# Kernel optimization log

Measured on AMD Instinct MI355X. Metric: run time of the kernel, lower is better.

Reference implementation:

```python
import jax, jax.numpy as jnp
import numpy as np

B, S, H, I, E, K = 2, 1024, 768, 1536, 8, 2
CAPACITY_FACTOR = 1.5
ROUTING_TEMP = 1.0
LB_WEIGHT = 0.001


def setup_inputs() -> dict:
    key = jax.random.key(0)
    k_x, k_g, k_w1, k_w3, k_w2 = jax.random.split(key, 5)
    std = 0.02
    return {
        "x": jax.random.normal(k_x, (B, S, H), dtype=jnp.float32),
        "w_gate": jax.random.normal(k_g, (H, E), dtype=jnp.float32) * 0.02,
        "w1": jax.random.normal(k_w1, (E, H, I), dtype=jnp.float32) * std,
        "w3": jax.random.normal(k_w3, (E, H, I), dtype=jnp.float32) * std,
        "w2": jax.random.normal(k_w2, (E, I, H), dtype=jnp.float32) * (std / np.sqrt(2 * 12)),
    }


def _moe_forward(x, w_gate, w1, w3, w2):
    Bb, Ss, Hh = x.shape
    T = Bb * Ss
    xf = x.reshape(T, Hh)

    # --- routing ---
    gate_logits = (xf @ w_gate) / ROUTING_TEMP          # [T, E]
    gate_probs = jax.nn.softmax(gate_logits, axis=-1)   # [T, E]
    topk_probs, topk_idx = jax.lax.top_k(gate_probs, K)  # [T, K]
    topk_probs = topk_probs / (topk_probs.sum(-1, keepdims=True) + 1e-8)

    # --- capacity dropping (per-k slot, token order, like the torch loop) ---
    capacity = max(8, int((T * K // E) * CAPACITY_FACTOR))
    onehot = (topk_idx[:, :, None] == jnp.arange(E)[None, None, :])  # [T, K, E] bool
    ranks = jnp.cumsum(onehot.astype(jnp.int32), axis=0)             # position of token in expert queue
    keep = onehot & (ranks <= capacity)                               # [T, K, E]

    # combine weight per (token, expert): sum over k of kept, clamped routing prob
    w_clamped = jnp.clip(topk_probs, 1e-8, 10.0)                      # [T, K]
    combine = jnp.einsum("tk,tke->te", w_clamped, keep.astype(xf.dtype))  # [T, E]

    # --- dense per-expert SwiGLU (reference form of masked dispatch) ---
    g = jnp.einsum("th,ehi->tei", xf, w1)   # [T, E, I]
    u = jnp.einsum("th,ehi->tei", xf, w3)   # [T, E, I]
    h = jax.nn.silu(g) * u                    # [T, E, I]
    y = jnp.einsum("tei,eih->teh", h, w2)   # [T, E, H]
    out = jnp.einsum("te,teh->th", combine, y).reshape(Bb, Ss, Hh)

    # --- load balancing loss ---
    expert_counts = keep.sum(axis=(0, 1)).astype(jnp.float32)         # [E]
    dropped = (onehot.sum() - keep.sum()).astype(jnp.float32)
    expert_usage = jax.lax.stop_gradient(expert_counts) / float(max(T * K, 1))
    gate_importance = gate_probs.mean(axis=0)                          # [E]
    aux = jnp.sum(expert_usage * gate_importance) * E
    aux = aux + jnp.where(dropped > 0, dropped / float(max(T, 1)) * 0.1, 0.0)
    aux = jnp.minimum(aux, 1.0) * LB_WEIGHT
    return out, aux


def reference(x, w_gate, w1, w3, w2):
    return _moe_forward(x, w_gate, w1, w3, w2)
```

## Files before the change

### kernel.cpp

```cpp
#include <hip/hip_runtime.h>
#include <math.h>

#define T_TOK 2048
#define HD 768
#define ID 1536
#define NE 8
#define CAP 768
#define TK 4096

typedef __bf16 bf16_t;
typedef __bf16 bf16x8 __attribute__((ext_vector_type(8)));
typedef __bf16 bf16x4 __attribute__((ext_vector_type(4)));
typedef float floatx4 __attribute__((ext_vector_type(4)));

__device__ __forceinline__ void gld16(const bf16_t* g, bf16_t* l) {
  __builtin_amdgcn_global_load_lds(
      (__attribute__((address_space(1))) void*)(g),
      (__attribute__((address_space(3))) void*)(l),
      16, 0, 0);
}

__global__ void k_route(const float* __restrict__ x, const float* __restrict__ wg,
                        bf16_t* __restrict__ xbf, int2* __restrict__ idx2,
                        float2* __restrict__ wc2, int2* __restrict__ tok_rows,
                        float* __restrict__ imp) {
  int t = blockIdx.x * 4 + (threadIdx.x >> 6);
  int lane = threadIdx.x & 63;
  const float* xr = x + (size_t)t * HD;
  int off = lane * 12;
  float4 a = *(const float4*)(xr + off);
  float4 b = *(const float4*)(xr + off + 4);
  float4 c = *(const float4*)(xr + off + 8);
  float xv[12] = {a.x, a.y, a.z, a.w, b.x, b.y, b.z, b.w, c.x, c.y, c.z, c.w};
  bf16x4 s0, s1, s2;
#pragma unroll
  for (int j = 0; j < 4; ++j) { s0[j] = (bf16_t)xv[j]; s1[j] = (bf16_t)xv[4 + j]; s2[j] = (bf16_t)xv[8 + j]; }
  bf16_t* xo = xbf + (size_t)t * HD + off;
  *(bf16x4*)xo = s0; *(bf16x4*)(xo + 4) = s1; *(bf16x4*)(xo + 8) = s2;

  float acc[8] = {0, 0, 0, 0, 0, 0, 0, 0};
#pragma unroll
  for (int jj = 0; jj < 12; ++jj) {
    const float4* wr = (const float4*)(wg + (size_t)(off + jj) * 8);
    float4 w0 = wr[0], w1 = wr[1];
    float v = xv[jj];
    acc[0] += v * w0.x; acc[1] += v * w0.y; acc[2] += v * w0.z; acc[3] += v * w0.w;
    acc[4] += v * w1.x; acc[5] += v * w1.y; acc[6] += v * w1.z; acc[7] += v * w1.w;
  }
#pragma unroll
  for (int e = 0; e < 8; ++e) {
    float v = acc[e];
    for (int s = 1; s < 64; s <<= 1) v += __shfl_xor(v, s, 64);
    acc[e] = v;
  }
  float mx = acc[0];
#pragma unroll
  for (int e = 1; e < 8; ++e) mx = fmaxf(mx, acc[e]);
  float p[8], sum = 0.f;
#pragma unroll
  for (int e = 0; e < 8; ++e) { p[e] = __expf(acc[e] - mx); sum += p[e]; }
#pragma unroll
  for (int e = 0; e < 8; ++e) p[e] /= sum;
  if (lane < 8) atomicAdd(&imp[lane], p[lane]);
  if (lane == 0) {
    int e0 = 0;
#pragma unroll
    for (int e = 1; e < 8; ++e) if (p[e] > p[e0]) e0 = e;
    int e1 = (e0 == 0) ? 1 : 0;
#pragma unroll
    for (int e = 0; e < 8; ++e) if (e != e0 && p[e] > p[e1]) e1 = e;
    float denom = p[e0] + p[e1] + 1e-8f;
    float w0c = fminf(fmaxf(p[e0] / denom, 1e-8f), 10.f);
    float w1c = fminf(fmaxf(p[e1] / denom, 1e-8f), 10.f);
    idx2[t] = make_int2(e0, e1);
    wc2[t] = make_float2(w0c, w1c);
    tok_rows[t] = make_int2(-1, -1);
  }
}

__global__ void k_scan(const int2* __restrict__ idx2, const float2* __restrict__ wc2,
                       const float* __restrict__ imp,
                       int* __restrict__ tok_of_row, float* __restrict__ wgt_of_row,
                       int2* __restrict__ tok_rows, int2* __restrict__ cnt_start,
                       float* __restrict__ aux_out) {
  __shared__ int sTot[16];
  __shared__ int sPos[8];
  int tid = threadIdx.x;
  int w = tid >> 6, lane = tid & 63;
  int s = w >> 3, e = w & 7;
  int t0 = lane * 32;
  int cnt = 0;
  for (int j = 0; j < 32; ++j) {
    int2 p = idx2[t0 + j];
    int ex = s ? p.y : p.x;
    cnt += (ex == e) ? 1 : 0;
  }
  int incl = cnt;
  for (int d = 1; d < 64; d <<= 1) {
    int v = __shfl_up(incl, d, 64);
    if (lane >= d) incl += v;
  }
  int excl = incl - cnt;
  if (lane == 63) sTot[w] = incl;
  __syncthreads();
  if (tid == 0) {
    int run = 0;
    float a = 0.f;
    for (int ee = 0; ee < 8; ++ee) {
      int k = min(sTot[ee], CAP) + min(sTot[8 + ee], CAP);
      sPos[ee] = run;
      cnt_start[ee] = make_int2(run, k);
      a += ((float)k / (float)TK) * (imp[ee] / (float)T_TOK);
      run += k;
    }
    a *= (float)NE;
    int dropped = TK - run;
    if (dropped > 0) a += (float)dropped / (float)T_TOK * 0.1f;
    a = fminf(a, 1.f) * 0.001f;
    aux_out[0] = a;
  }
  __syncthreads();
  int rank = excl;
  for (int j = 0; j < 32; ++j) {
    int t = t0 + j;
    int2 p = idx2[t];
    int ex = s ? p.y : p.x;
    if (ex == e) {
      rank++;
      if (rank <= CAP) {
        int pos = atomicAdd(&sPos[e], 1);
        tok_of_row[pos] = t;
        float2 wv = wc2[t];
        wgt_of_row[pos] = s ? wv.y : wv.x;
        ((int*)tok_rows)[2 * t + s] = pos;
      }
    }
  }
}

__global__ void k_tr(const float* __restrict__ w1, const float* __restrict__ w3,
                     const float* __restrict__ w2, bf16_t* __restrict__ w1t,
                     bf16_t* __restrict__ w3t, bf16_t* __restrict__ w2t) {
  __shared__ bf16_t tl[64][65];
  int z = blockIdx.z;
  const float* src; bf16_t* dst; int R, C, r0, c0;
  if (z < 16) {
    R = HD; C = ID; r0 = blockIdx.y * 64; c0 = blockIdx.x * 64;
    int e = z & 7;
    if (z < 8) { src = w1 + (size_t)e * R * C; dst = w1t + (size_t)e * R * C; }
    else       { src = w3 + (size_t)e * R * C; dst = w3t + (size_t)e * R * C; }
  } else {
    R = ID; C = HD; r0 = blockIdx.x * 64; c0 = blockIdx.y * 64;
    int e = z - 16;
    src = w2 + (size_t)e * R * C; dst = w2t + (size_t)e * R * C;
  }
  int tid = threadIdx.x;
  int lr = tid >> 2, lc = (tid & 3) * 16;
  const float* sp = src + (size_t)(r0 + lr) * C + c0 + lc;
#pragma unroll
  for (int j = 0; j < 16; j += 4) {
    float4 v = *(const float4*)(sp + j);
    tl[lr][lc + j + 0] = (bf16_t)v.x;
    tl[lr][lc + j + 1] = (bf16_t)v.y;
    tl[lr][lc + j + 2] = (bf16_t)v.z;
    tl[lr][lc + j + 3] = (bf16_t)v.w;
  }
  __syncthreads();
  int oc = tid >> 2, orr = (tid & 3) * 16;
  bf16_t* d = dst + (size_t)(c0 + oc) * R + r0 + orr;
  bf16x8 v0, v1;
#pragma unroll
  for (int j = 0; j < 8; ++j) v0[j] = tl[orr + j][oc];
#pragma unroll
  for (int j = 0; j < 8; ++j) v1[j] = tl[orr + 8 + j][oc];
  *(bf16x8*)d = v0;
  *(bf16x8*)(d + 8) = v1;
}

__global__ __launch_bounds__(256, 3)
void k_gemm1(const bf16_t* __restrict__ xbf, const bf16_t* __restrict__ w1t,
             const bf16_t* __restrict__ w3t, const int* __restrict__ tok_of_row,
             const int2* __restrict__ cnt_start, bf16_t* __restrict__ h_ws) {
  int e = blockIdx.x & 7, j = blockIdx.x >> 3;
  int2 cs = cnt_start[e];
  int nrows = cs.y - j * 128;
  if (nrows <= 0) return;
  if (nrows > 128) nrows = 128;
  int grow0 = cs.x + j * 128;
  int cy = blockIdx.y;

  __shared__ __attribute__((aligned(16))) bf16_t Abuf[128 * 32];
  __shared__ __attribute__((aligned(16))) bf16_t B1buf[64 * 32];
  __shared__ __attribute__((aligned(16))) bf16_t B3buf[64 * 32];

  int tid = threadIdx.x;
  int lane = tid & 63, wv = tid >> 6;
  int wm = wv & 1, wn = wv >> 1;
  int lr = lane & 15, q = lane >> 4;
  int rdc = (q ^ ((lane >> 1) & 3)) * 8;
  int srow = lane >> 2;
  int gch = ((lane & 3) ^ ((lane >> 3) & 3)) * 8;

  int ra = wv * 32 + srow;
  int tokA0 = tok_of_row[grow0 + min(ra, nrows - 1)];
  int tokA1 = tok_of_row[grow0 + min(ra + 16, nrows - 1)];
  const bf16_t* gA0 = xbf + (size_t)tokA0 * HD + gch;
  const bf16_t* gA1 = xbf + (size_t)tokA1 * HD + gch;
  int nb = cy * 64 + wv * 16 + srow;
  const bf16_t* gB1 = w1t + ((size_t)e * ID + nb) * HD + gch;
  const bf16_t* gB3 = w3t + ((size_t)e * ID + nb) * HD + gch;
  bf16_t* lA0 = &Abuf[(wv * 32) * 32];
  bf16_t* lA1 = &Abuf[(wv * 32 + 16) * 32];
  bf16_t* lB1 = &B1buf[(wv * 16) * 32];
  bf16_t* lB3 = &B3buf[(wv * 16) * 32];

  floatx4 accg[4][2] = {};
  floatx4 accu[4][2] = {};

  for (int kk = 0; kk < 24; ++kk) {
    __syncthreads();
    gld16(gA0, lA0); gld16(gA1, lA1);
    gld16(gB1, lB1); gld16(gB3, lB3);
    gA0 += 32; gA1 += 32; gB1 += 32; gB3 += 32;
    __syncthreads();
    bf16x8 af[4], b1f[2], b3f[2];
#pragma unroll
    for (int i = 0; i < 4; ++i) af[i] = *(const bf16x8*)&Abuf[(wm * 64 + i * 16 + lr) * 32 + rdc];
#pragma unroll
    for (int i = 0; i < 2; ++i) b1f[i] = *(const bf16x8*)&B1buf[(wn * 32 + i * 16 + lr) * 32 + rdc];
#pragma unroll
    for (int i = 0; i < 2; ++i) b3f[i] = *(const bf16x8*)&B3buf[(wn * 32 + i * 16 + lr) * 32 + rdc];
#pragma unroll
    for (int i = 0; i < 4; ++i)
#pragma unroll
      for (int jj = 0; jj < 2; ++jj) {
        accg[i][jj] = __builtin_amdgcn_mfma_f32_16x16x32_bf16(af[i], b1f[jj], accg[i][jj], 0, 0, 0);
        accu[i][jj] = __builtin_amdgcn_mfma_f32_16x16x32_bf16(af[i], b3f[jj], accu[i][jj], 0, 0, 0);
      }
  }
#pragma unroll
  for (int i = 0; i < 4; ++i)
#pragma unroll
    for (int r = 0; r < 4; ++r) {
      int rl = wm * 64 + i * 16 + q * 4 + r;
      if (rl < nrows) {
        size_t rb = (size_t)(grow0 + rl) * ID + cy * 64 + wn * 32 + lr;
#pragma unroll
        for (int jj = 0; jj < 2; ++jj) {
          float gg = accg[i][jj][r], uu = accu[i][jj][r];
          float sg = gg / (1.f + __expf(-gg));
          h_ws[rb + jj * 16] = (bf16_t)(sg * uu);
        }
      }
    }
}

__global__ __launch_bounds__(256, 4)
void k_gemm2(const bf16_t* __restrict__ h_ws, const bf16_t* __restrict__ w2t,
             const int* __restrict__ tok_of_row, const float* __restrict__ wgt_of_row,
             const int2* __restrict__ cnt_start, float* __restrict__ out) {
  int e = blockIdx.x & 7, j = blockIdx.x >> 3;
  int2 cs = cnt_start[e];
  int nrows = cs.y - j * 128;
  if (nrows <= 0) return;
  if (nrows > 128) nrows = 128;
  int grow0 = cs.x + j * 128;
  int cy = blockIdx.y;

  __shared__ __attribute__((aligned(16))) bf16_t Abuf[128 * 32];
  __shared__ __attribute__((aligned(16))) bf16_t Bbuf[64 * 32];

  int tid = threadIdx.x;
  int lane = tid & 63, wv = tid >> 6;
  int wm = wv & 1, wn = wv >> 1;
  int lr = lane & 15, q = lane >> 4;
  int rdc = (q ^ ((lane >> 1) & 3)) * 8;
  int srow = lane >> 2;
  int gch = ((lane & 3) ^ ((lane >> 3) & 3)) * 8;

  int ra = wv * 32 + srow;
  const bf16_t* gA0 = h_ws + (size_t)(grow0 + min(ra, nrows - 1)) * ID + gch;
  const bf16_t* gA1 = h_ws + (size_t)(grow0 + min(ra + 16, nrows - 1)) * ID + gch;
  int nb = cy * 64 + wv * 16 + srow;
  const bf16_t* gB = w2t + ((size_t)e * HD + nb) * ID + gch;
  bf16_t* lA0 = &Abuf[(wv * 32) * 32];
  bf16_t* lA1 = &Abuf[(wv * 32 + 16) * 32];
  bf16_t* lB = &Bbuf[(wv * 16) * 32];

  floatx4 acc[4][2] = {};

  for (int kk = 0; kk < 48; ++kk) {
    __syncthreads();
    gld16(gA0, lA0); gld16(gA1, lA1);
    gld16(gB, lB);
    gA0 += 32; gA1 += 32; gB += 32;
    __syncthreads();
    bf16x8 af[4], bfr[2];
#pragma unroll
    for (int i = 0; i < 4; ++i) af[i] = *(const bf16x8*)&Abuf[(wm * 64 + i * 16 + lr) * 32 + rdc];
#pragma unroll
    for (int i = 0; i < 2; ++i) bfr[i] = *(const bf16x8*)&Bbuf[(wn * 32 + i * 16 + lr) * 32 + rdc];
#pragma unroll
    for (int i = 0; i < 4; ++i)
#pragma unroll
      for (int jj = 0; jj < 2; ++jj)
        acc[i][jj] = __builtin_amdgcn_mfma_f32_16x16x32_bf16(af[i], bfr[jj], acc[i][jj], 0, 0, 0);
  }
#pragma unroll
  for (int i = 0; i < 4; ++i)
#pragma unroll
    for (int r = 0; r < 4; ++r) {
      int rl = wm * 64 + i * 16 + q * 4 + r;
      if (rl < nrows) {
        int grow = grow0 + rl;
        int tok = tok_of_row[grow];
        float wgt = wgt_of_row[grow];
        size_t ob = (size_t)tok * HD + cy * 64 + wn * 32 + lr;
#pragma unroll
        for (int jj = 0; jj < 2; ++jj)
          atomicAdd(&out[ob + jj * 16], wgt * acc[i][jj][r]);
      }
    }
}

extern "C" void kernel_launch(void* const* d_in, const int* in_sizes, int n_in,
                              void* d_out, int out_size, void* d_ws, size_t ws_size,
                              hipStream_t stream) {
  const float* x  = (const float*)d_in[0];
  const float* wg = (const float*)d_in[1];
  const float* w1 = (const float*)d_in[2];
  const float* w3 = (const float*)d_in[3];
  const float* w2 = (const float*)d_in[4];
  float* out = (float*)d_out;

  char* ws = (char*)d_ws;
  bf16_t* xbf  = (bf16_t*)(ws + 0);
  bf16_t* w1t  = (bf16_t*)(ws + 3145728);
  bf16_t* w3t  = (bf16_t*)(ws + 22020096);
  bf16_t* w2t  = (bf16_t*)(ws + 40894464);
  bf16_t* h_ws = (bf16_t*)(ws + 59768832);
  int2*   idx2 = (int2*)(ws + 72351744);
  float2* wc2  = (float2*)(ws + 72368128);
  int*    tok_of_row = (int*)(ws + 72384512);
  float*  wgt_of_row = (float*)(ws + 72400896);
  int2*   tok_rows   = (int2*)(ws + 72417280);
  int2*   cnt_start  = (int2*)(ws + 72433664);
  float*  imp        = (float*)(ws + 72433728);

  float* aux_out = out + (size_t)T_TOK * HD;

  hipMemsetAsync(out, 0, (size_t)T_TOK * HD * sizeof(float), stream);
  hipMemsetAsync(imp, 0, NE * sizeof(float), stream);
  k_route<<<512, 256, 0, stream>>>(x, wg, xbf, idx2, wc2, tok_rows, imp);
  k_scan<<<1, 1024, 0, stream>>>(idx2, wc2, imp, tok_of_row, wgt_of_row,
                                 tok_rows, cnt_start, aux_out);
  k_tr<<<dim3(24, 12, 24), 256, 0, stream>>>(w1, w3, w2, w1t, w3t, w2t);
  k_gemm1<<<dim3(96, 24), 256, 0, stream>>>(xbf, w1t, w3t, tok_of_row,
                                            cnt_start, h_ws);
  k_gemm2<<<dim3(96, 12), 256, 0, stream>>>(h_ws, w2t, tok_of_row, wgt_of_row,
                                            cnt_start, out);
}
```

Before: 288.7 us.

## Fuse weight fp32-to-bf16 conversion into GEMMs with weight-stationary LDS tiles

Removes the separate transpose/convert kernel and its bf16 weight buffers. Each GEMM block now loads a 16-column slice of one expert's fp32 weights straight from global memory, converts it, and keeps the full K-depth in swizzled LDS. It then streams all of that expert's token rows through it, reading A fragments directly from global memory into registers with double-buffering. This cuts a full pass over the weights and a launch, but the wave count per expert is low and A rows are re-read once per column slice. The GEMM2 epilogue also issues more scattered atomics.

```diff
diff --git a/kernel.cpp b/kernel.cpp
--- a/kernel.cpp
+++ b/kernel.cpp
@@ -13,17 +13,9 @@
 typedef __bf16 bf16x4 __attribute__((ext_vector_type(4)));
 typedef float floatx4 __attribute__((ext_vector_type(4)));
 
-__device__ __forceinline__ void gld16(const bf16_t* g, bf16_t* l) {
-  __builtin_amdgcn_global_load_lds(
-      (__attribute__((address_space(1))) void*)(g),
-      (__attribute__((address_space(3))) void*)(l),
-      16, 0, 0);
-}
-
 __global__ void k_route(const float* __restrict__ x, const float* __restrict__ wg,
                         bf16_t* __restrict__ xbf, int2* __restrict__ idx2,
-                        float2* __restrict__ wc2, int2* __restrict__ tok_rows,
-                        float* __restrict__ imp) {
+                        float2* __restrict__ wc2, float* __restrict__ imp) {
   int t = blockIdx.x * 4 + (threadIdx.x >> 6);
   int lane = threadIdx.x & 63;
   const float* xr = x + (size_t)t * HD;
@@ -74,15 +66,13 @@
     float w1c = fminf(fmaxf(p[e1] / denom, 1e-8f), 10.f);
     idx2[t] = make_int2(e0, e1);
     wc2[t] = make_float2(w0c, w1c);
-    tok_rows[t] = make_int2(-1, -1);
   }
 }
 
 __global__ void k_scan(const int2* __restrict__ idx2, const float2* __restrict__ wc2,
                        const float* __restrict__ imp,
                        int* __restrict__ tok_of_row, float* __restrict__ wgt_of_row,
-                       int2* __restrict__ tok_rows, int2* __restrict__ cnt_start,
-                       float* __restrict__ aux_out) {
+                       int2* __restrict__ cnt_start, float* __restrict__ aux_out) {
   __shared__ int sTot[16];
   __shared__ int sPos[8];
   int tid = threadIdx.x;
@@ -132,195 +122,196 @@
         tok_of_row[pos] = t;
         float2 wv = wc2[t];
         wgt_of_row[pos] = s ? wv.y : wv.x;
-        ((int*)tok_rows)[2 * t + s] = pos;
-      }
-    }
-  }
-}
-
-__global__ void k_tr(const float* __restrict__ w1, const float* __restrict__ w3,
-                     const float* __restrict__ w2, bf16_t* __restrict__ w1t,
-                     bf16_t* __restrict__ w3t, bf16_t* __restrict__ w2t) {
-  __shared__ bf16_t tl[64][65];
-  int z = blockIdx.z;
-  const float* src; bf16_t* dst; int R, C, r0, c0;
-  if (z < 16) {
-    R = HD; C = ID; r0 = blockIdx.y * 64; c0 = blockIdx.x * 64;
-    int e = z & 7;
-    if (z < 8) { src = w1 + (size_t)e * R * C; dst = w1t + (size_t)e * R * C; }
-    else       { src = w3 + (size_t)e * R * C; dst = w3t + (size_t)e * R * C; }
-  } else {
-    R = ID; C = HD; r0 = blockIdx.x * 64; c0 = blockIdx.y * 64;
-    int e = z - 16;
-    src = w2 + (size_t)e * R * C; dst = w2t + (size_t)e * R * C;
-  }
+      }
+    }
+  }
+}
+
+__global__ __launch_bounds__(256, 3)
+void k_gemm1(const bf16_t* __restrict__ xbf, const float* __restrict__ w1,
+             const float* __restrict__ w3, const int* __restrict__ tok_of_row,
+             const int2* __restrict__ cnt_start, bf16_t* __restrict__ h_ws) {
+  int e = blockIdx.x & 7, cy = blockIdx.x >> 3;
+  int n0 = cy * 16;
+  int2 cs = cnt_start[e];
+  int nrows = cs.y;
+  if (nrows <= 0) return;
+  int grow0 = cs.x;
+
+  __shared__ __attribute__((aligned(16))) bf16_t BL[2][24 * 512];
+
   int tid = threadIdx.x;
-  int lr = tid >> 2, lc = (tid & 3) * 16;
-  const float* sp = src + (size_t)(r0 + lr) * C + c0 + lc;
-#pragma unroll
-  for (int j = 0; j < 16; j += 4) {
-    float4 v = *(const float4*)(sp + j);
-    tl[lr][lc + j + 0] = (bf16_t)v.x;
-    tl[lr][lc + j + 1] = (bf16_t)v.y;
-    tl[lr][lc + j + 2] = (bf16_t)v.z;
-    tl[lr][lc + j + 3] = (bf16_t)v.w;
+  {
+    int i4 = (tid & 3) * 4;
+    int hb = (tid >> 2) * 12;
+    const float* s1 = w1 + ((size_t)e * HD + hb) * ID + n0 + i4;
+    const float* s3 = w3 + ((size_t)e * HD + hb) * ID + n0 + i4;
+    for (int hh = 0; hh < 12; ++hh) {
+      int h = hb + hh;
+      int kc = h >> 5, kin = h & 31;
+      int c8 = kin >> 3, kb = kin & 7;
+      float4 v1 = *(const float4*)(s1 + (size_t)hh * ID);
+      float4 v3 = *(const float4*)(s3 + (size_t)hh * ID);
+      float a1[4] = {v1.x, v1.y, v1.z, v1.w};
+      float a3[4] = {v3.x, v3.y, v3.z, v3.w};
+#pragma unroll
+      for (int c = 0; c < 4; ++c) {
+        int n = i4 + c;
+        int p = c8 ^ ((n >> 1) & 3);
+        int idx = kc * 512 + n * 32 + p * 8 + kb;
+        BL[0][idx] = (bf16_t)a1[c];
+        BL[1][idx] = (bf16_t)a3[c];
+      }
+    }
   }
   __syncthreads();
-  int oc = tid >> 2, orr = (tid & 3) * 16;
-  bf16_t* d = dst + (size_t)(c0 + oc) * R + r0 + orr;
-  bf16x8 v0, v1;
-#pragma unroll
-  for (int j = 0; j < 8; ++j) v0[j] = tl[orr + j][oc];
-#pragma unroll
-  for (int j = 0; j < 8; ++j) v1[j] = tl[orr + 8 + j][oc];
-  *(bf16x8*)d = v0;
-  *(bf16x8*)(d + 8) = v1;
+
+  int lane = tid & 63, w = tid >> 6;
+  int lr = lane & 15, q = lane >> 4;
+  int boff = lr * 32 + (q ^ ((lr >> 1) & 3)) * 8;
+
+  int njt = (nrows + 255) >> 8;
+  for (int j = 0; j < njt; ++j) {
+    int rbase = j * 256 + w * 64;
+    const bf16_t* ap[4];
+#pragma unroll
+    for (int mf = 0; mf < 4; ++mf) {
+      int tok = tok_of_row[grow0 + min(rbase + mf * 16 + lr, nrows - 1)];
+      ap[mf] = xbf + (size_t)tok * HD + q * 8;
+    }
+    floatx4 accg[4] = {};
+    floatx4 accu[4] = {};
+    bf16x8 a[2][2][4], b1[2][2], b3[2][2];
+#pragma unroll
+    for (int cc = 0; cc < 2; ++cc) {
+#pragma unroll
+      for (int mf = 0; mf < 4; ++mf) a[0][cc][mf] = *(const bf16x8*)(ap[mf] + cc * 32);
+      b1[0][cc] = *(const bf16x8*)&BL[0][cc * 512 + boff];
+      b3[0][cc] = *(const bf16x8*)&BL[1][cc * 512 + boff];
+    }
+#pragma unroll
+    for (int u = 0; u < 12; ++u) {
+      int s = u & 1;
+      if (u < 11) {
+        int kc0 = (u + 1) * 2;
+#pragma unroll
+        for (int cc = 0; cc < 2; ++cc) {
+#pragma unroll
+          for (int mf = 0; mf < 4; ++mf)
+            a[s ^ 1][cc][mf] = *(const bf16x8*)(ap[mf] + (size_t)(kc0 + cc) * 32);
+          b1[s ^ 1][cc] = *(const bf16x8*)&BL[0][(kc0 + cc) * 512 + boff];
+          b3[s ^ 1][cc] = *(const bf16x8*)&BL[1][(kc0 + cc) * 512 + boff];
+        }
+      }
+#pragma unroll
+      for (int cc = 0; cc < 2; ++cc)
+#pragma unroll
+        for (int mf = 0; mf < 4; ++mf) {
+          accg[mf] = __builtin_amdgcn_mfma_f32_16x16x32_bf16(a[s][cc][mf], b1[s][cc], accg[mf], 0, 0, 0);
+          accu[mf] = __builtin_amdgcn_mfma_f32_16x16x32_bf16(a[s][cc][mf], b3[s][cc], accu[mf], 0, 0, 0);
+        }
+    }
+#pragma unroll
+    for (int mf = 0; mf < 4; ++mf)
+#pragma unroll
+      for (int rr = 0; rr < 4; ++rr) {
+        int r = rbase + mf * 16 + q * 4 + rr;
+        if (r < nrows) {
+          float gg = accg[mf][rr], uu = accu[mf][rr];
+          float sg = gg / (1.f + __expf(-gg));
+          h_ws[(size_t)(grow0 + r) * ID + n0 + lr] = (bf16_t)(sg * uu);
+        }
+      }
+  }
 }
 
 __global__ __launch_bounds__(256, 3)
-void k_gemm1(const bf16_t* __restrict__ xbf, const bf16_t* __restrict__ w1t,
-             const bf16_t* __restrict__ w3t, const int* __restrict__ tok_of_row,
-             const int2* __restrict__ cnt_start, bf16_t* __restrict__ h_ws) {
-  int e = blockIdx.x & 7, j = blockIdx.x >> 3;
-  int2 cs = cnt_start[e];
-  int nrows = cs.y - j * 128;
-  if (nrows <= 0) return;
-  if (nrows > 128) nrows = 128;
-  int grow0 = cs.x + j * 128;
-  int cy = blockIdx.y;
-
-  __shared__ __attribute__((aligned(16))) bf16_t Abuf[128 * 32];
-  __shared__ __attribute__((aligned(16))) bf16_t B1buf[64 * 32];
-  __shared__ __attribute__((aligned(16))) bf16_t B3buf[64 * 32];
-
-  int tid = threadIdx.x;
-  int lane = tid & 63, wv = tid >> 6;
-  int wm = wv & 1, wn = wv >> 1;
-  int lr = lane & 15, q = lane >> 4;
-  int rdc = (q ^ ((lane >> 1) & 3)) * 8;
-  int srow = lane >> 2;
-  int gch = ((lane & 3) ^ ((lane >> 3) & 3)) * 8;
-
-  int ra = wv * 32 + srow;
-  int tokA0 = tok_of_row[grow0 + min(ra, nrows - 1)];
-  int tokA1 = tok_of_row[grow0 + min(ra + 16, nrows - 1)];
-  const bf16_t* gA0 = xbf + (size_t)tokA0 * HD + gch;
-  const bf16_t* gA1 = xbf + (size_t)tokA1 * HD + gch;
-  int nb = cy * 64 + wv * 16 + srow;
-  const bf16_t* gB1 = w1t + ((size_t)e * ID + nb) * HD + gch;
-  const bf16_t* gB3 = w3t + ((size_t)e * ID + nb) * HD + gch;
-  bf16_t* lA0 = &Abuf[(wv * 32) * 32];
-  bf16_t* lA1 = &Abuf[(wv * 32 + 16) * 32];
-  bf16_t* lB1 = &B1buf[(wv * 16) * 32];
-  bf16_t* lB3 = &B3buf[(wv * 16) * 32];
-
-  floatx4 accg[4][2] = {};
-  floatx4 accu[4][2] = {};
-
-  for (int kk = 0; kk < 24; ++kk) {
-    __syncthreads();
-    gld16(gA0, lA0); gld16(gA1, lA1);
-    gld16(gB1, lB1); gld16(gB3, lB3);
-    gA0 += 32; gA1 += 32; gB1 += 32; gB3 += 32;
-    __syncthreads();
-    bf16x8 af[4], b1f[2], b3f[2];
-#pragma unroll
-    for (int i = 0; i < 4; ++i) af[i] = *(const bf16x8*)&Abuf[(wm * 64 + i * 16 + lr) * 32 + rdc];
-#pragma unroll
-    for (int i = 0; i < 2; ++i) b1f[i] = *(const bf16x8*)&B1buf[(wn * 32 + i * 16 + lr) * 32 + rdc];
-#pragma unroll
-    for (int i = 0; i < 2; ++i) b3f[i] = *(const bf16x8*)&B3buf[(wn * 32 + i * 16 + lr) * 32 + rdc];
-#pragma unroll
-    for (int i = 0; i < 4; ++i)
-#pragma unroll
-      for (int jj = 0; jj < 2; ++jj) {
-        accg[i][jj] = __builtin_amdgcn_mfma_f32_16x16x32_bf16(af[i], b1f[jj], accg[i][jj], 0, 0, 0);
-        accu[i][jj] = __builtin_amdgcn_mfma_f32_16x16x32_bf16(af[i], b3f[jj], accu[i][jj], 0, 0, 0);
-      }
-  }
-#pragma unroll
-  for (int i = 0; i < 4; ++i)
-#pragma unroll
-    for (int r = 0; r < 4; ++r) {
-      int rl = wm * 64 + i * 16 + q * 4 + r;
-      if (rl < nrows) {
-        size_t rb = (size_t)(grow0 + rl) * ID + cy * 64 + wn * 32 + lr;
-#pragma unroll
-        for (int jj = 0; jj < 2; ++jj) {
-          float gg = accg[i][jj][r], uu = accu[i][jj][r];
-          float sg = gg / (1.f + __expf(-gg));
-          h_ws[rb + jj * 16] = (bf16_t)(sg * uu);
-        }
-      }
-    }
-}
-
-__global__ __launch_bounds__(256, 4)
-void k_gemm2(const bf16_t* __restrict__ h_ws, const bf16_t* __restrict__ w2t,
+void k_gemm2(const bf16_t* __restrict__ h_ws, const float* __restrict__ w2,
              const int* __restrict__ tok_of_row, const float* __restrict__ wgt_of_row,
              const int2* __restrict__ cnt_start, float* __restrict__ out) {
-  int e = blockIdx.x & 7, j = blockIdx.x >> 3;
+  int e = blockIdx.x & 7, ch = blockIdx.x >> 3;
+  int n0 = ch * 16;
   int2 cs = cnt_start[e];
-  int nrows = cs.y - j * 128;
+  int nrows = cs.y;
   if (nrows <= 0) return;
-  if (nrows > 128) nrows = 128;
-  int grow0 = cs.x + j * 128;
-  int cy = blockIdx.y;
-
-  __shared__ __attribute__((aligned(16))) bf16_t Abuf[128 * 32];
-  __shared__ __attribute__((aligned(16))) bf16_t Bbuf[64 * 32];
+  int grow0 = cs.x;
+
+  __shared__ __attribute__((aligned(16))) bf16_t BL[48 * 512];
 
   int tid = threadIdx.x;
-  int lane = tid & 63, wv = tid >> 6;
-  int wm = wv & 1, wn = wv >> 1;
+  {
+    int n4 = (tid & 3) * 4;
+    int ib = (tid >> 2) * 24;
+    const float* s2 = w2 + ((size_t)e * ID + ib) * HD + n0 + n4;
+    for (int ii = 0; ii < 24; ++ii) {
+      int i = ib + ii;
+      int kc = i >> 5, kin = i & 31;
+      int c8 = kin >> 3, kb = kin & 7;
+      float4 v = *(const float4*)(s2 + (size_t)ii * HD);
+      float av[4] = {v.x, v.y, v.z, v.w};
+#pragma unroll
+      for (int c = 0; c < 4; ++c) {
+        int n = n4 + c;
+        int p = c8 ^ ((n >> 1) & 3);
+        BL[kc * 512 + n * 32 + p * 8 + kb] = (bf16_t)av[c];
+      }
+    }
+  }
+  __syncthreads();
+
+  int lane = tid & 63, w = tid >> 6;
   int lr = lane & 15, q = lane >> 4;
-  int rdc = (q ^ ((lane >> 1) & 3)) * 8;
-  int srow = lane >> 2;
-  int gch = ((lane & 3) ^ ((lane >> 3) & 3)) * 8;
-
-  int ra = wv * 32 + srow;
-  const bf16_t* gA0 = h_ws + (size_t)(grow0 + min(ra, nrows - 1)) * ID + gch;
-  const bf16_t* gA1 = h_ws + (size_t)(grow0 + min(ra + 16, nrows - 1)) * ID + gch;
-  int nb = cy * 64 + wv * 16 + srow;
-  const bf16_t* gB = w2t + ((size_t)e * HD + nb) * ID + gch;
-  bf16_t* lA0 = &Abuf[(wv * 32) * 32];
-  bf16_t* lA1 = &Abuf[(wv * 32 + 16) * 32];
-  bf16_t* lB = &Bbuf[(wv * 16) * 32];
-
-  floatx4 acc[4][2] = {};
-
-  for (int kk = 0; kk < 48; ++kk) {
-    __syncthreads();
-    gld16(gA0, lA0); gld16(gA1, lA1);
-    gld16(gB, lB);
-    gA0 += 32; gA1 += 32; gB += 32;
-    __syncthreads();
-    bf16x8 af[4], bfr[2];
-#pragma unroll
-    for (int i = 0; i < 4; ++i) af[i] = *(const bf16x8*)&Abuf[(wm * 64 + i * 16 + lr) * 32 + rdc];
-#pragma unroll
-    for (int i = 0; i < 2; ++i) bfr[i] = *(const bf16x8*)&Bbuf[(wn * 32 + i * 16 + lr) * 32 + rdc];
-#pragma unroll
-    for (int i = 0; i < 4; ++i)
-#pragma unroll
-      for (int jj = 0; jj < 2; ++jj)
-        acc[i][jj] = __builtin_amdgcn_mfma_f32_16x16x32_bf16(af[i], bfr[jj], acc[i][jj], 0, 0, 0);
-  }
-#pragma unroll
-  for (int i = 0; i < 4; ++i)
-#pragma unroll
-    for (int r = 0; r < 4; ++r) {
-      int rl = wm * 64 + i * 16 + q * 4 + r;
-      if (rl < nrows) {
-        int grow = grow0 + rl;
-        int tok = tok_of_row[grow];
-        float wgt = wgt_of_row[grow];
-        size_t ob = (size_t)tok * HD + cy * 64 + wn * 32 + lr;
-#pragma unroll
-        for (int jj = 0; jj < 2; ++jj)
-          atomicAdd(&out[ob + jj * 16], wgt * acc[i][jj][r]);
-      }
-    }
+  int boff = lr * 32 + (q ^ ((lr >> 1) & 3)) * 8;
+
+  int njt = (nrows + 255) >> 8;
+  for (int j = 0; j < njt; ++j) {
+    int rbase = j * 256 + w * 64;
+    const bf16_t* ap[4];
+#pragma unroll
+    for (int mf = 0; mf < 4; ++mf) {
+      int row = grow0 + min(rbase + mf * 16 + lr, nrows - 1);
+      ap[mf] = h_ws + (size_t)row * ID + q * 8;
+    }
+    floatx4 acc[4] = {};
+    bf16x8 a[2][2][4], bb[2][2];
+#pragma unroll
+    for (int cc = 0; cc < 2; ++cc) {
+#pragma unroll
+      for (int mf = 0; mf < 4; ++mf) a[0][cc][mf] = *(const bf16x8*)(ap[mf] + cc * 32);
+      bb[0][cc] = *(const bf16x8*)&BL[cc * 512 + boff];
+    }
+#pragma unroll
+    for (int u = 0; u < 24; ++u) {
+      int s = u & 1;
+      if (u < 23) {
+        int kc0 = (u + 1) * 2;
+#pragma unroll
+        for (int cc = 0; cc < 2; ++cc) {
+#pragma unroll
+          for (int mf = 0; mf < 4; ++mf)
+            a[s ^ 1][cc][mf] = *(const bf16x8*)(ap[mf] + (size_t)(kc0 + cc) * 32);
+          bb[s ^ 1][cc] = *(const bf16x8*)&BL[(kc0 + cc) * 512 + boff];
+        }
+      }
+#pragma unroll
+      for (int cc = 0; cc < 2; ++cc)
+#pragma unroll
+        for (int mf = 0; mf < 4; ++mf)
+          acc[mf] = __builtin_amdgcn_mfma_f32_16x16x32_bf16(a[s][cc][mf], bb[s][cc], acc[mf], 0, 0, 0);
+    }
+#pragma unroll
+    for (int mf = 0; mf < 4; ++mf)
+#pragma unroll
+      for (int rr = 0; rr < 4; ++rr) {
+        int r = rbase + mf * 16 + q * 4 + rr;
+        if (r < nrows) {
+          int grow = grow0 + r;
+          int tok = tok_of_row[grow];
+          float wgt = wgt_of_row[grow];
+          atomicAdd(&out[(size_t)tok * HD + n0 + lr], wgt * acc[mf][rr]);
+        }
+      }
+  }
 }
 
 extern "C" void kernel_launch(void* const* d_in, const int* in_sizes, int n_in,
@@ -335,28 +326,22 @@
 
   char* ws = (char*)d_ws;
   bf16_t* xbf  = (bf16_t*)(ws + 0);
-  bf16_t* w1t  = (bf16_t*)(ws + 3145728);
-  bf16_t* w3t  = (bf16_t*)(ws + 22020096);
-  bf16_t* w2t  = (bf16_t*)(ws + 40894464);
-  bf16_t* h_ws = (bf16_t*)(ws + 59768832);
-  int2*   idx2 = (int2*)(ws + 72351744);
-  float2* wc2  = (float2*)(ws + 72368128);
-  int*    tok_of_row = (int*)(ws + 72384512);
-  float*  wgt_of_row = (float*)(ws + 72400896);
-  int2*   tok_rows   = (int2*)(ws + 72417280);
-  int2*   cnt_start  = (int2*)(ws + 72433664);
-  float*  imp        = (float*)(ws + 72433728);
+  bf16_t* h_ws = (bf16_t*)(ws + 3145728);
+  int2*   idx2 = (int2*)(ws + 15728640);
+  float2* wc2  = (float2*)(ws + 15745024);
+  int*    tok_of_row = (int*)(ws + 15761408);
+  float*  wgt_of_row = (float*)(ws + 15777792);
+  int2*   cnt_start  = (int2*)(ws + 15794176);
+  float*  imp        = (float*)(ws + 15794240);
 
   float* aux_out = out + (size_t)T_TOK * HD;
 
   hipMemsetAsync(out, 0, (size_t)T_TOK * HD * sizeof(float), stream);
   hipMemsetAsync(imp, 0, NE * sizeof(float), stream);
-  k_route<<<512, 256, 0, stream>>>(x, wg, xbf, idx2, wc2, tok_rows, imp);
+  k_route<<<512, 256, 0, stream>>>(x, wg, xbf, idx2, wc2, imp);
   k_scan<<<1, 1024, 0, stream>>>(idx2, wc2, imp, tok_of_row, wgt_of_row,
-                                 tok_rows, cnt_start, aux_out);
-  k_tr<<<dim3(24, 12, 24), 256, 0, stream>>>(w1, w3, w2, w1t, w3t, w2t);
-  k_gemm1<<<dim3(96, 24), 256, 0, stream>>>(xbf, w1t, w3t, tok_of_row,
-                                            cnt_start, h_ws);
-  k_gemm2<<<dim3(96, 12), 256, 0, stream>>>(h_ws, w2t, tok_of_row, wgt_of_row,
-                                            cnt_start, out);
-}
+                                 cnt_start, aux_out);
+  k_gemm1<<<768, 256, 0, stream>>>(xbf, w1, w3, tok_of_row, cnt_start, h_ws);
+  k_gemm2<<<384, 256, 0, stream>>>(h_ws, w2, tok_of_row, wgt_of_row,
+                                   cnt_start, out);
+}
```

Result: slower. 482.9 us (+67.2%).

## Fuse routing, output zeroing and weight conversion into one prep kernel with tiled weight layout

Applied to the files above, without the earlier changes.

Merges the routing kernel, the output memset and the weight transpose kernel into one launch. Weights are now converted to bf16 in a pre-tiled, pre-swizzled per-(expert, n-block, k-chunk) layout, so each GEMM block streams contiguous 4 KB chunks. Importance is computed from stored probabilities in the scan kernel instead of global atomics, and the scan stages indices in shared memory. GEMM grids become 1D with n-block-major ordering, and gemm1 occupancy hint rises to 4. The prep conversion blocks now loop over many k-chunks serially, which may lengthen the tail of that kernel.

```diff
diff --git a/kernel.cpp b/kernel.cpp
--- a/kernel.cpp
+++ b/kernel.cpp
@@ -7,6 +7,11 @@
 #define NE 8
 #define CAP 768
 #define TK 4096
+#define RT 12
+#define NB1 24
+#define KC1 24
+#define NB2 12
+#define KC2 48
 
 typedef __bf16 bf16_t;
 typedef __bf16 bf16x8 __attribute__((ext_vector_type(8)));
@@ -20,80 +25,151 @@
       16, 0, 0);
 }
 
-__global__ void k_route(const float* __restrict__ x, const float* __restrict__ wg,
-                        bf16_t* __restrict__ xbf, int2* __restrict__ idx2,
-                        float2* __restrict__ wc2, int2* __restrict__ tok_rows,
-                        float* __restrict__ imp) {
-  int t = blockIdx.x * 4 + (threadIdx.x >> 6);
-  int lane = threadIdx.x & 63;
-  const float* xr = x + (size_t)t * HD;
-  int off = lane * 12;
-  float4 a = *(const float4*)(xr + off);
-  float4 b = *(const float4*)(xr + off + 4);
-  float4 c = *(const float4*)(xr + off + 8);
-  float xv[12] = {a.x, a.y, a.z, a.w, b.x, b.y, b.z, b.w, c.x, c.y, c.z, c.w};
-  bf16x4 s0, s1, s2;
-#pragma unroll
-  for (int j = 0; j < 4; ++j) { s0[j] = (bf16_t)xv[j]; s1[j] = (bf16_t)xv[4 + j]; s2[j] = (bf16_t)xv[8 + j]; }
-  bf16_t* xo = xbf + (size_t)t * HD + off;
-  *(bf16x4*)xo = s0; *(bf16x4*)(xo + 4) = s1; *(bf16x4*)(xo + 8) = s2;
-
-  float acc[8] = {0, 0, 0, 0, 0, 0, 0, 0};
-#pragma unroll
-  for (int jj = 0; jj < 12; ++jj) {
-    const float4* wr = (const float4*)(wg + (size_t)(off + jj) * 8);
-    float4 w0 = wr[0], w1 = wr[1];
-    float v = xv[jj];
-    acc[0] += v * w0.x; acc[1] += v * w0.y; acc[2] += v * w0.z; acc[3] += v * w0.w;
-    acc[4] += v * w1.x; acc[5] += v * w1.y; acc[6] += v * w1.z; acc[7] += v * w1.w;
-  }
-#pragma unroll
-  for (int e = 0; e < 8; ++e) {
-    float v = acc[e];
-    for (int s = 1; s < 64; s <<= 1) v += __shfl_xor(v, s, 64);
-    acc[e] = v;
-  }
-  float mx = acc[0];
-#pragma unroll
-  for (int e = 1; e < 8; ++e) mx = fmaxf(mx, acc[e]);
-  float p[8], sum = 0.f;
-#pragma unroll
-  for (int e = 0; e < 8; ++e) { p[e] = __expf(acc[e] - mx); sum += p[e]; }
-#pragma unroll
-  for (int e = 0; e < 8; ++e) p[e] /= sum;
-  if (lane < 8) atomicAdd(&imp[lane], p[lane]);
-  if (lane == 0) {
-    int e0 = 0;
-#pragma unroll
-    for (int e = 1; e < 8; ++e) if (p[e] > p[e0]) e0 = e;
-    int e1 = (e0 == 0) ? 1 : 0;
-#pragma unroll
-    for (int e = 0; e < 8; ++e) if (e != e0 && p[e] > p[e1]) e1 = e;
-    float denom = p[e0] + p[e1] + 1e-8f;
-    float w0c = fminf(fmaxf(p[e0] / denom, 1e-8f), 10.f);
-    float w1c = fminf(fmaxf(p[e1] / denom, 1e-8f), 10.f);
-    idx2[t] = make_int2(e0, e1);
-    wc2[t] = make_float2(w0c, w1c);
-    tok_rows[t] = make_int2(-1, -1);
+__global__ void k_prep(const float* __restrict__ x, const float* __restrict__ wg,
+                       const float* __restrict__ w1, const float* __restrict__ w3,
+                       const float* __restrict__ w2,
+                       bf16_t* __restrict__ xbf, bf16_t* __restrict__ w1b,
+                       bf16_t* __restrict__ w3b, bf16_t* __restrict__ w2b,
+                       int2* __restrict__ idx2, float2* __restrict__ wc2,
+                       float* __restrict__ probs8, float* __restrict__ outz) {
+  int b = blockIdx.x;
+  int tid = threadIdx.x;
+  if (b < 512) {
+#pragma unroll
+    for (int k2 = 0; k2 < 3; ++k2) {
+      float4 z = make_float4(0.f, 0.f, 0.f, 0.f);
+      *(float4*)(outz + (size_t)b * 3072 + k2 * 1024 + tid * 4) = z;
+    }
+    int t = b * 4 + (tid >> 6);
+    int lane = tid & 63;
+    const float* xr = x + (size_t)t * HD;
+    int off = lane * 12;
+    float4 a = *(const float4*)(xr + off);
+    float4 bv = *(const float4*)(xr + off + 4);
+    float4 c = *(const float4*)(xr + off + 8);
+    float xv[12] = {a.x, a.y, a.z, a.w, bv.x, bv.y, bv.z, bv.w, c.x, c.y, c.z, c.w};
+    bf16x4 s0, s1, s2;
+#pragma unroll
+    for (int j = 0; j < 4; ++j) { s0[j] = (bf16_t)xv[j]; s1[j] = (bf16_t)xv[4 + j]; s2[j] = (bf16_t)xv[8 + j]; }
+    bf16_t* xo = xbf + (size_t)t * HD + off;
+    *(bf16x4*)xo = s0; *(bf16x4*)(xo + 4) = s1; *(bf16x4*)(xo + 8) = s2;
+
+    float acc[8] = {0, 0, 0, 0, 0, 0, 0, 0};
+#pragma unroll
+    for (int jj = 0; jj < 12; ++jj) {
+      const float4* wr = (const float4*)(wg + (size_t)(off + jj) * 8);
+      float4 w0 = wr[0], w1v = wr[1];
+      float v = xv[jj];
+      acc[0] += v * w0.x; acc[1] += v * w0.y; acc[2] += v * w0.z; acc[3] += v * w0.w;
+      acc[4] += v * w1v.x; acc[5] += v * w1v.y; acc[6] += v * w1v.z; acc[7] += v * w1v.w;
+    }
+#pragma unroll
+    for (int e = 0; e < 8; ++e) {
+      float v = acc[e];
+      for (int s = 1; s < 64; s <<= 1) v += __shfl_xor(v, s, 64);
+      acc[e] = v;
+    }
+    float mx = acc[0];
+#pragma unroll
+    for (int e = 1; e < 8; ++e) mx = fmaxf(mx, acc[e]);
+    float p[8], sum = 0.f;
+#pragma unroll
+    for (int e = 0; e < 8; ++e) { p[e] = __expf(acc[e] - mx); sum += p[e]; }
+#pragma unroll
+    for (int e = 0; e < 8; ++e) p[e] /= sum;
+    if (lane == 0) {
+      float4 P0 = make_float4(p[0], p[1], p[2], p[3]);
+      float4 P1 = make_float4(p[4], p[5], p[6], p[7]);
+      *(float4*)&probs8[t * 8] = P0;
+      *(float4*)&probs8[t * 8 + 4] = P1;
+      int e0 = 0;
+#pragma unroll
+      for (int e = 1; e < 8; ++e) if (p[e] > p[e0]) e0 = e;
+      int e1 = (e0 == 0) ? 1 : 0;
+#pragma unroll
+      for (int e = 0; e < 8; ++e) if (e != e0 && p[e] > p[e1]) e1 = e;
+      float denom = p[e0] + p[e1] + 1e-8f;
+      float w0c = fminf(fmaxf(p[e0] / denom, 1e-8f), 10.f);
+      float w1c = fminf(fmaxf(p[e1] / denom, 1e-8f), 10.f);
+      idx2[t] = make_int2(e0, e1);
+      wc2[t] = make_float2(w0c, w1c);
+    }
+  } else {
+    __shared__ bf16_t sm[32 * 68];
+    int ib = b - 512;
+    const float* src; bf16_t* dst; int C, KC;
+    if (ib < 192) {
+      int e = ib & 7, nb = ib >> 3;
+      src = w1 + (size_t)e * HD * ID + nb * 64;
+      dst = w1b + (size_t)((e * NB1 + nb) * KC1) * 2048;
+      C = ID; KC = KC1;
+    } else if (ib < 384) {
+      int e = (ib - 192) & 7, nb = (ib - 192) >> 3;
+      src = w3 + (size_t)e * HD * ID + nb * 64;
+      dst = w3b + (size_t)((e * NB1 + nb) * KC1) * 2048;
+      C = ID; KC = KC1;
+    } else {
+      int e = (ib - 384) & 7, nb = (ib - 384) >> 3;
+      src = w2 + (size_t)e * ID * HD + nb * 64;
+      dst = w2b + (size_t)((e * NB2 + nb) * KC2) * 2048;
+      C = HD; KC = KC2;
+    }
+    int r = tid >> 3, t7 = tid & 7;
+    int n = tid >> 2, pch = tid & 3;
+    int cl = pch ^ ((n >> 1) & 3);
+    for (int kc = 0; kc < KC; ++kc) {
+      const float* sp = src + (size_t)(kc * 32 + r) * C + t7 * 8;
+      float4 va = *(const float4*)sp;
+      float4 vb = *(const float4*)(sp + 4);
+      bf16x4 ba, bb;
+      ba[0] = (bf16_t)va.x; ba[1] = (bf16_t)va.y; ba[2] = (bf16_t)va.z; ba[3] = (bf16_t)va.w;
+      bb[0] = (bf16_t)vb.x; bb[1] = (bf16_t)vb.y; bb[2] = (bf16_t)vb.z; bb[3] = (bf16_t)vb.w;
+      *(bf16x4*)&sm[r * 68 + t7 * 8] = ba;
+      *(bf16x4*)&sm[r * 68 + t7 * 8 + 4] = bb;
+      __syncthreads();
+      bf16x8 o;
+#pragma unroll
+      for (int j = 0; j < 8; ++j) o[j] = sm[(cl * 8 + j) * 68 + n];
+      *(bf16x8*)(dst + (size_t)kc * 2048 + tid * 8) = o;
+      __syncthreads();
+    }
   }
 }
 
 __global__ void k_scan(const int2* __restrict__ idx2, const float2* __restrict__ wc2,
-                       const float* __restrict__ imp,
+                       const float* __restrict__ probs8,
                        int* __restrict__ tok_of_row, float* __restrict__ wgt_of_row,
-                       int2* __restrict__ tok_rows, int2* __restrict__ cnt_start,
-                       float* __restrict__ aux_out) {
+                       int2* __restrict__ cnt_start, float* __restrict__ aux_out) {
+  __shared__ int2 sIdx[2048];
+  __shared__ float2 sWc[2048];
   __shared__ int sTot[16];
   __shared__ int sPos[8];
+  __shared__ float sImp[16][8];
   int tid = threadIdx.x;
+  sIdx[tid] = idx2[tid]; sIdx[tid + 1024] = idx2[tid + 1024];
+  sWc[tid] = wc2[tid];  sWc[tid + 1024] = wc2[tid + 1024];
+  const float4* pp = (const float4*)probs8;
+  float4 u0 = pp[tid * 4], u1 = pp[tid * 4 + 1], u2 = pp[tid * 4 + 2], u3 = pp[tid * 4 + 3];
+  float im[8] = {u0.x + u2.x, u0.y + u2.y, u0.z + u2.z, u0.w + u2.w,
+                 u1.x + u3.x, u1.y + u3.y, u1.z + u3.z, u1.w + u3.w};
+#pragma unroll
+  for (int e = 0; e < 8; ++e) {
+    float v = im[e];
+    for (int d = 1; d < 64; d <<= 1) v += __shfl_xor(v, d, 64);
+    im[e] = v;
+  }
   int w = tid >> 6, lane = tid & 63;
+  if (lane == 0) {
+#pragma unroll
+    for (int e = 0; e < 8; ++e) sImp[w][e] = im[e];
+  }
+  __syncthreads();
   int s = w >> 3, e = w & 7;
   int t0 = lane * 32;
   int cnt = 0;
   for (int j = 0; j < 32; ++j) {
-    int2 p = idx2[t0 + j];
-    int ex = s ? p.y : p.x;
-    cnt += (ex == e) ? 1 : 0;
+    int2 p = sIdx[t0 + j];
+    cnt += ((s ? p.y : p.x) == e) ? 1 : 0;
   }
   int incl = cnt;
   for (int d = 1; d < 64; d <<= 1) {
@@ -104,90 +180,51 @@
   if (lane == 63) sTot[w] = incl;
   __syncthreads();
   if (tid == 0) {
-    int run = 0;
-    float a = 0.f;
+    int run = 0; float a = 0.f;
     for (int ee = 0; ee < 8; ++ee) {
+      float impv = 0.f;
+      for (int ww = 0; ww < 16; ++ww) impv += sImp[ww][ee];
       int k = min(sTot[ee], CAP) + min(sTot[8 + ee], CAP);
       sPos[ee] = run;
       cnt_start[ee] = make_int2(run, k);
-      a += ((float)k / (float)TK) * (imp[ee] / (float)T_TOK);
+      a += ((float)k / (float)TK) * (impv / (float)T_TOK);
       run += k;
     }
     a *= (float)NE;
     int dropped = TK - run;
     if (dropped > 0) a += (float)dropped / (float)T_TOK * 0.1f;
-    a = fminf(a, 1.f) * 0.001f;
-    aux_out[0] = a;
+    aux_out[0] = fminf(a, 1.f) * 0.001f;
   }
   __syncthreads();
   int rank = excl;
   for (int j = 0; j < 32; ++j) {
     int t = t0 + j;
-    int2 p = idx2[t];
+    int2 p = sIdx[t];
     int ex = s ? p.y : p.x;
     if (ex == e) {
       rank++;
       if (rank <= CAP) {
         int pos = atomicAdd(&sPos[e], 1);
         tok_of_row[pos] = t;
-        float2 wv = wc2[t];
+        float2 wv = sWc[t];
         wgt_of_row[pos] = s ? wv.y : wv.x;
-        ((int*)tok_rows)[2 * t + s] = pos;
       }
     }
   }
 }
 
-__global__ void k_tr(const float* __restrict__ w1, const float* __restrict__ w3,
-                     const float* __restrict__ w2, bf16_t* __restrict__ w1t,
-                     bf16_t* __restrict__ w3t, bf16_t* __restrict__ w2t) {
-  __shared__ bf16_t tl[64][65];
-  int z = blockIdx.z;
-  const float* src; bf16_t* dst; int R, C, r0, c0;
-  if (z < 16) {
-    R = HD; C = ID; r0 = blockIdx.y * 64; c0 = blockIdx.x * 64;
-    int e = z & 7;
-    if (z < 8) { src = w1 + (size_t)e * R * C; dst = w1t + (size_t)e * R * C; }
-    else       { src = w3 + (size_t)e * R * C; dst = w3t + (size_t)e * R * C; }
-  } else {
-    R = ID; C = HD; r0 = blockIdx.x * 64; c0 = blockIdx.y * 64;
-    int e = z - 16;
-    src = w2 + (size_t)e * R * C; dst = w2t + (size_t)e * R * C;
-  }
-  int tid = threadIdx.x;
-  int lr = tid >> 2, lc = (tid & 3) * 16;
-  const float* sp = src + (size_t)(r0 + lr) * C + c0 + lc;
-#pragma unroll
-  for (int j = 0; j < 16; j += 4) {
-    float4 v = *(const float4*)(sp + j);
-    tl[lr][lc + j + 0] = (bf16_t)v.x;
-    tl[lr][lc + j + 1] = (bf16_t)v.y;
-    tl[lr][lc + j + 2] = (bf16_t)v.z;
-    tl[lr][lc + j + 3] = (bf16_t)v.w;
-  }
-  __syncthreads();
-  int oc = tid >> 2, orr = (tid & 3) * 16;
-  bf16_t* d = dst + (size_t)(c0 + oc) * R + r0 + orr;
-  bf16x8 v0, v1;
-#pragma unroll
-  for (int j = 0; j < 8; ++j) v0[j] = tl[orr + j][oc];
-#pragma unroll
-  for (int j = 0; j < 8; ++j) v1[j] = tl[orr + 8 + j][oc];
-  *(bf16x8*)d = v0;
-  *(bf16x8*)(d + 8) = v1;
-}
-
-__global__ __launch_bounds__(256, 3)
-void k_gemm1(const bf16_t* __restrict__ xbf, const bf16_t* __restrict__ w1t,
-             const bf16_t* __restrict__ w3t, const int* __restrict__ tok_of_row,
+__global__ __launch_bounds__(256, 4)
+void k_gemm1(const bf16_t* __restrict__ xbf, const bf16_t* __restrict__ w1b,
+             const bf16_t* __restrict__ w3b, const int* __restrict__ tok_of_row,
              const int2* __restrict__ cnt_start, bf16_t* __restrict__ h_ws) {
-  int e = blockIdx.x & 7, j = blockIdx.x >> 3;
+  int e = blockIdx.x & 7;
+  int t = blockIdx.x >> 3;
+  int nb = t / RT, rt = t - nb * RT;
   int2 cs = cnt_start[e];
-  int nrows = cs.y - j * 128;
+  int nrows = cs.y - rt * 128;
   if (nrows <= 0) return;
   if (nrows > 128) nrows = 128;
-  int grow0 = cs.x + j * 128;
-  int cy = blockIdx.y;
+  int grow0 = cs.x + rt * 128;
 
   __shared__ __attribute__((aligned(16))) bf16_t Abuf[128 * 32];
   __shared__ __attribute__((aligned(16))) bf16_t B1buf[64 * 32];
@@ -206,22 +243,21 @@
   int tokA1 = tok_of_row[grow0 + min(ra + 16, nrows - 1)];
   const bf16_t* gA0 = xbf + (size_t)tokA0 * HD + gch;
   const bf16_t* gA1 = xbf + (size_t)tokA1 * HD + gch;
-  int nb = cy * 64 + wv * 16 + srow;
-  const bf16_t* gB1 = w1t + ((size_t)e * ID + nb) * HD + gch;
-  const bf16_t* gB3 = w3t + ((size_t)e * ID + nb) * HD + gch;
+  const bf16_t* p1 = w1b + (size_t)((e * NB1 + nb) * KC1) * 2048 + tid * 8;
+  const bf16_t* p3 = w3b + (size_t)((e * NB1 + nb) * KC1) * 2048 + tid * 8;
   bf16_t* lA0 = &Abuf[(wv * 32) * 32];
   bf16_t* lA1 = &Abuf[(wv * 32 + 16) * 32];
-  bf16_t* lB1 = &B1buf[(wv * 16) * 32];
-  bf16_t* lB3 = &B3buf[(wv * 16) * 32];
+  bf16_t* lB1 = &B1buf[wv * 512];
+  bf16_t* lB3 = &B3buf[wv * 512];
 
   floatx4 accg[4][2] = {};
   floatx4 accu[4][2] = {};
 
-  for (int kk = 0; kk < 24; ++kk) {
+  for (int kk = 0; kk < KC1; ++kk) {
     __syncthreads();
     gld16(gA0, lA0); gld16(gA1, lA1);
-    gld16(gB1, lB1); gld16(gB3, lB3);
-    gA0 += 32; gA1 += 32; gB1 += 32; gB3 += 32;
+    gld16(p1, lB1); gld16(p3, lB3);
+    gA0 += 32; gA1 += 32; p1 += 2048; p3 += 2048;
     __syncthreads();
     bf16x8 af[4], b1f[2], b3f[2];
 #pragma unroll
@@ -244,7 +280,7 @@
     for (int r = 0; r < 4; ++r) {
       int rl = wm * 64 + i * 16 + q * 4 + r;
       if (rl < nrows) {
-        size_t rb = (size_t)(grow0 + rl) * ID + cy * 64 + wn * 32 + lr;
+        size_t rb = (size_t)(grow0 + rl) * ID + nb * 64 + wn * 32 + lr;
 #pragma unroll
         for (int jj = 0; jj < 2; ++jj) {
           float gg = accg[i][jj][r], uu = accu[i][jj][r];
@@ -256,16 +292,17 @@
 }
 
 __global__ __launch_bounds__(256, 4)
-void k_gemm2(const bf16_t* __restrict__ h_ws, const bf16_t* __restrict__ w2t,
+void k_gemm2(const bf16_t* __restrict__ h_ws, const bf16_t* __restrict__ w2b,
              const int* __restrict__ tok_of_row, const float* __restrict__ wgt_of_row,
              const int2* __restrict__ cnt_start, float* __restrict__ out) {
-  int e = blockIdx.x & 7, j = blockIdx.x >> 3;
+  int e = blockIdx.x & 7;
+  int t = blockIdx.x >> 3;
+  int nb = t / RT, rt = t - nb * RT;
   int2 cs = cnt_start[e];
-  int nrows = cs.y - j * 128;
+  int nrows = cs.y - rt * 128;
   if (nrows <= 0) return;
   if (nrows > 128) nrows = 128;
-  int grow0 = cs.x + j * 128;
-  int cy = blockIdx.y;
+  int grow0 = cs.x + rt * 128;
 
   __shared__ __attribute__((aligned(16))) bf16_t Abuf[128 * 32];
   __shared__ __attribute__((aligned(16))) bf16_t Bbuf[64 * 32];
@@ -281,19 +318,18 @@
   int ra = wv * 32 + srow;
   const bf16_t* gA0 = h_ws + (size_t)(grow0 + min(ra, nrows - 1)) * ID + gch;
   const bf16_t* gA1 = h_ws + (size_t)(grow0 + min(ra + 16, nrows - 1)) * ID + gch;
-  int nb = cy * 64 + wv * 16 + srow;
-  const bf16_t* gB = w2t + ((size_t)e * HD + nb) * ID + gch;
+  const bf16_t* pB = w2b + (size_t)((e * NB2 + nb) * KC2) * 2048 + tid * 8;
   bf16_t* lA0 = &Abuf[(wv * 32) * 32];
   bf16_t* lA1 = &Abuf[(wv * 32 + 16) * 32];
-  bf16_t* lB = &Bbuf[(wv * 16) * 32];
+  bf16_t* lB = &Bbuf[wv * 512];
 
   floatx4 acc[4][2] = {};
 
-  for (int kk = 0; kk < 48; ++kk) {
+  for (int kk = 0; kk < KC2; ++kk) {
     __syncthreads();
     gld16(gA0, lA0); gld16(gA1, lA1);
-    gld16(gB, lB);
-    gA0 += 32; gA1 += 32; gB += 32;
+    gld16(pB, lB);
+    gA0 += 32; gA1 += 32; pB += 2048;
     __syncthreads();
     bf16x8 af[4], bfr[2];
 #pragma unroll
@@ -315,7 +351,7 @@
         int grow = grow0 + rl;
         int tok = tok_of_row[grow];
         float wgt = wgt_of_row[grow];
-        size_t ob = (size_t)tok * HD + cy * 64 + wn * 32 + lr;
+        size_t ob = (size_t)tok * HD + nb * 64 + wn * 32 + lr;
 #pragma unroll
         for (int jj = 0; jj < 2; ++jj)
           atomicAdd(&out[ob + jj * 16], wgt * acc[i][jj][r]);
@@ -335,28 +371,25 @@
 
   char* ws = (char*)d_ws;
   bf16_t* xbf  = (bf16_t*)(ws + 0);
-  bf16_t* w1t  = (bf16_t*)(ws + 3145728);
-  bf16_t* w3t  = (bf16_t*)(ws + 22020096);
-  bf16_t* w2t  = (bf16_t*)(ws + 40894464);
+  bf16_t* w1b  = (bf16_t*)(ws + 3145728);
+  bf16_t* w3b  = (bf16_t*)(ws + 22020096);
+  bf16_t* w2b  = (bf16_t*)(ws + 40894464);
   bf16_t* h_ws = (bf16_t*)(ws + 59768832);
-  int2*   idx2 = (int2*)(ws + 72351744);
-  float2* wc2  = (float2*)(ws + 72368128);
-  int*    tok_of_row = (int*)(ws + 72384512);
-  float*  wgt_of_row = (float*)(ws + 72400896);
-  int2*   tok_rows   = (int2*)(ws + 72417280);
-  int2*   cnt_start  = (int2*)(ws + 72433664);
-  float*  imp        = (float*)(ws + 72433728);
+  float*  probs8     = (float*)(ws + 72351744);
+  int2*   idx2       = (int2*)(ws + 72417280);
+  float2* wc2        = (float2*)(ws + 72433664);
+  int*    tok_of_row = (int*)(ws + 72450048);
+  float*  wgt_of_row = (float*)(ws + 72466432);
+  int2*   cnt_start  = (int2*)(ws + 72482816);
 
   float* aux_out = out + (size_t)T_TOK * HD;
 
-  hipMemsetAsync(out, 0, (size_t)T_TOK * HD * sizeof(float), stream);
-  hipMemsetAsync(imp, 0, NE * sizeof(float), stream);
-  k_route<<<512, 256, 0, stream>>>(x, wg, xbf, idx2, wc2, tok_rows, imp);
-  k_scan<<<1, 1024, 0, stream>>>(idx2, wc2, imp, tok_of_row, wgt_of_row,
-                                 tok_rows, cnt_start, aux_out);
-  k_tr<<<dim3(24, 12, 24), 256, 0, stream>>>(w1, w3, w2, w1t, w3t, w2t);
-  k_gemm1<<<dim3(96, 24), 256, 0, stream>>>(xbf, w1t, w3t, tok_of_row,
+  k_prep<<<992, 256, 0, stream>>>(x, wg, w1, w3, w2, xbf, w1b, w3b, w2b,
+                                  idx2, wc2, probs8, out);
+  k_scan<<<1, 1024, 0, stream>>>(idx2, wc2, probs8, tok_of_row, wgt_of_row,
+                                 cnt_start, aux_out);
+  k_gemm1<<<8 * NB1 * RT, 256, 0, stream>>>(xbf, w1b, w3b, tok_of_row,
                                             cnt_start, h_ws);
-  k_gemm2<<<dim3(96, 12), 256, 0, stream>>>(h_ws, w2t, tok_of_row, wgt_of_row,
+  k_gemm2<<<8 * NB2 * RT, 256, 0, stream>>>(h_ws, w2b, tok_of_row, wgt_of_row,
                                             cnt_start, out);
 }
```

New measurement: 277.8 us. 1.04x faster.
